# Optimization experiments

Hardware: AMD Instinct MI355X
Metric: run time of the kernel (lower is better)

The kernel has to match this reference:

```python
import jax, jax.numpy as jnp
import numpy as np

TEMPERATURE = 0.05
SINKHORN_ITERS = 10


def setup_inputs() -> dict:
    key = jax.random.key(0)
    ks = jax.random.split(key, 6)
    N, D, E = 4096, 300, 32768
    x = jax.random.normal(ks[0], (N, D), dtype=jnp.float32)
    W1 = jax.random.normal(ks[1], (D, D), dtype=jnp.float32) * 0.05
    b1 = jax.random.normal(ks[2], (D,), dtype=jnp.float32) * 0.01
    W2 = jax.random.normal(ks[3], (D, D), dtype=jnp.float32) * 0.05
    b2 = jax.random.normal(ks[4], (D,), dtype=jnp.float32) * 0.01
    edge_index = jax.random.randint(ks[5], (2, E), 0, N, dtype=jnp.int64)
    return {"x": x, "W1": W1, "b1": b1, "W2": W2, "b2": b2,
            "edge_index": edge_index}


def _sinkhorn(dot):
    # dot: [N, N]; batch dim of 1 in the original collapses away.
    in_size = dot.shape[0]
    out_size = dot.shape[1]
    K = jnp.exp(dot)
    v = jnp.ones((out_size,), dtype=K.dtype)
    a = jnp.asarray(out_size / in_size, dtype=K.dtype)
    u = jnp.ones((in_size,), dtype=K.dtype)
    for _ in range(SINKHORN_ITERS):
        u = a / (K @ v)            # [N]
        v = 1.0 / (u @ K)          # [N]
    return u[:, None] * (K * v[None, :])  # [N, N] coupling


def reference(x, W1, b1, W2, b2, edge_index):
    N = x.shape[0]
    # projector: Linear -> ReLU -> Linear
    out = jax.nn.relu(x @ W1 + b1) @ W2 + b2
    # L2 normalize rows (torch F.normalize with eps=1e-12)
    norm = jnp.maximum(jnp.linalg.norm(out, axis=1, keepdims=True), 1e-12)
    node_features = out / norm
    logits = (node_features @ node_features.T) / TEMPERATURE  # [N, N]
    log_probs = jax.nn.log_softmax(logits, axis=1)
    # Sinkhorn coupling computed under no_grad in the original
    coupling = jax.lax.stop_gradient(_sinkhorn(logits))
    loss = -jnp.mean(jnp.sum(coupling * log_probs, axis=1))
    # dense 2-hop adjacency target
    src, dst = edge_index[0], edge_index[1]
    adj = jnp.zeros((N, N), dtype=jnp.float32).at[src, dst].set(1.0)
    adj = adj + jnp.eye(N, dtype=jnp.float32)
    adj2 = ((adj @ adj) > 0).astype(jnp.float32)
    targets = adj2 / jnp.sum(adj2, axis=0, keepdims=True)
    loss = loss + (-jnp.mean(jnp.sum(targets * log_probs, axis=1)))
    return loss
```

## Files before the change

### kernel.cpp

```cpp
#include <hip/hip_runtime.h>
#include <cstdint>
#include <cstddef>

#define N 4096
#define D 300
#define KP 320
#define INV_T 20.0f
#define SK_ITERS 10
#define NTILE 528

typedef __attribute__((ext_vector_type(8))) short bf16x8;
typedef __attribute__((ext_vector_type(4))) float f32x4;
typedef __attribute__((ext_vector_type(8))) unsigned short ushort8;

__device__ inline void tile_decode(int blk, int& bi, int& bj) {
  int lin = (blk & 7) * 66 + (blk >> 3);
  int a = 0;
  while (lin >= 32 - a) { lin -= 32 - a; ++a; }
  bi = a; bj = a + lin;
}

__global__ void zero_u32(unsigned int* __restrict__ p, int n) {
  int i = blockIdx.x * 256 + threadIdx.x;
  int stride = gridDim.x * 256;
  for (; i < n; i += stride) p[i] = 0u;
}

__global__ __launch_bounds__(320) void mlp_gemm(const float* __restrict__ A,
                                                const float* __restrict__ B,
                                                const float* __restrict__ bias,
                                                float* __restrict__ C, int relu) {
  __shared__ __align__(16) float As[4][304];
  int r0 = blockIdx.x * 4;
  for (int idx = threadIdx.x; idx < 4 * 300; idx += 320) {
    int r = idx / 300, k = idx - r * 300;
    As[r][k] = A[(size_t)(r0 + r) * D + k];
  }
  __syncthreads();
  int c = threadIdx.x;
  if (c < D) {
    float acc[4] = {0, 0, 0, 0};
    for (int k = 0; k < D; k += 4) {
      float b0 = B[(size_t)(k + 0) * D + c];
      float b1 = B[(size_t)(k + 1) * D + c];
      float b2 = B[(size_t)(k + 2) * D + c];
      float b3 = B[(size_t)(k + 3) * D + c];
#pragma unroll
      for (int r = 0; r < 4; ++r) {
        const float4 a4 = *reinterpret_cast<const float4*>(&As[r][k]);
        acc[r] += a4.x * b0 + a4.y * b1 + a4.z * b2 + a4.w * b3;
      }
    }
#pragma unroll
    for (int r = 0; r < 4; ++r) {
      float o = acc[r] + bias[c];
      if (relu) o = fmaxf(o, 0.0f);
      C[(size_t)(r0 + r) * D + c] = o;
    }
  }
}

__device__ inline unsigned short bf16_rne(float v) {
  unsigned int u = __float_as_uint(v);
  unsigned int r = u + 0x7fffu + ((u >> 16) & 1u);
  return (unsigned short)(r >> 16);
}

__global__ __launch_bounds__(64) void normalize_split(const float* __restrict__ in,
                                                      unsigned short* __restrict__ fhi,
                                                      unsigned short* __restrict__ flo) {
  int row = blockIdx.x;
  const float* r = in + (size_t)row * D;
  float ss = 0.0f;
  for (int c = threadIdx.x; c < D; c += 64) {
    float v = r[c];
    ss += v * v;
  }
  for (int o = 32; o > 0; o >>= 1) ss += __shfl_down(ss, o);
  ss = __shfl(ss, 0);
  float inv = 1.0f / fmaxf(sqrtf(ss), 1e-12f);
  for (int c = threadIdx.x; c < KP; c += 64) {
    float v = (c < D) ? r[c] * inv : 0.0f;
    unsigned short h = bf16_rne(v);
    float hf = __uint_as_float((unsigned int)h << 16);
    unsigned short lo = bf16_rne(v - hf);
    fhi[(size_t)row * KP + c] = h;
    flo[(size_t)row * KP + c] = lo;
  }
}

__global__ __launch_bounds__(256) void logits_mfma(const unsigned short* __restrict__ fhi,
                                                   const unsigned short* __restrict__ flo,
                                                   float* __restrict__ logits) {
  __shared__ unsigned short smem[4 * 128 * 32];
  int bi, bj;
  tile_decode(blockIdx.x, bi, bj);
  int row0 = bi * 128, col0 = bj * 128;
  int tid = threadIdx.x;
  int w = tid >> 6, l = tid & 63;
  int wr = w >> 1, wc = w & 1;
  f32x4 acc[4][4] = {};

  for (int k0 = 0; k0 < KP; k0 += 32) {
    ushort8 stg[8];
#pragma unroll
    for (int t = 0; t < 8; ++t) {
      int c = t * 256 + tid;
      int b = c >> 9, i = c & 511, row = i >> 2, k16 = i & 3;
      const unsigned short* base = (b & 1) ? flo : fhi;
      int blk = (b < 2) ? row0 : col0;
      stg[t] = *reinterpret_cast<const ushort8*>(
          &base[(size_t)(blk + row) * KP + k0 + k16 * 8]);
    }
    __syncthreads();
#pragma unroll
    for (int t = 0; t < 8; ++t) {
      int c = t * 256 + tid;
      *reinterpret_cast<ushort8*>(&smem[c * 8]) = stg[t];
    }
    __syncthreads();

    bf16x8 ah[4], al[4], bh[4], bl[4];
#pragma unroll
    for (int m = 0; m < 4; ++m) {
      int off = (wr * 64 + m * 16 + (l & 15)) * 32 + (l >> 4) * 8;
      ah[m] = *reinterpret_cast<const bf16x8*>(&smem[0 * 4096 + off]);
      al[m] = *reinterpret_cast<const bf16x8*>(&smem[1 * 4096 + off]);
    }
#pragma unroll
    for (int n = 0; n < 4; ++n) {
      int off = (wc * 64 + n * 16 + (l & 15)) * 32 + (l >> 4) * 8;
      bh[n] = *reinterpret_cast<const bf16x8*>(&smem[2 * 4096 + off]);
      bl[n] = *reinterpret_cast<const bf16x8*>(&smem[3 * 4096 + off]);
    }
#pragma unroll
    for (int m = 0; m < 4; ++m)
#pragma unroll
      for (int n = 0; n < 4; ++n) {
        acc[m][n] = __builtin_amdgcn_mfma_f32_16x16x32_bf16(ah[m], bh[n], acc[m][n], 0, 0, 0);
        acc[m][n] = __builtin_amdgcn_mfma_f32_16x16x32_bf16(ah[m], bl[n], acc[m][n], 0, 0, 0);
        acc[m][n] = __builtin_amdgcn_mfma_f32_16x16x32_bf16(al[m], bh[n], acc[m][n], 0, 0, 0);
      }
  }

  int rb = row0 + wr * 64, cb = col0 + wc * 64;
  int rsub = (l >> 4) * 4, csub = l & 15;
#pragma unroll
  for (int m = 0; m < 4; ++m) {
#pragma unroll
    for (int n = 0; n < 4; ++n) {
      int col = cb + n * 16 + csub;
#pragma unroll
      for (int j = 0; j < 4; ++j) {
        logits[(size_t)(rb + m * 16 + rsub + j) * N + col] = acc[m][n][j] * INV_T;
      }
    }
  }
}

__global__ __launch_bounds__(256) void sk_tile(const float* __restrict__ logits,
                                               const float* __restrict__ vin,
                                               float* __restrict__ pr) {
  __shared__ float red[16][8][17];
  int bi, bj;
  tile_decode(blockIdx.x, bi, bj);
  int row0 = bi * 128, col0 = bj * 128;
  int t = threadIdx.x, ty = t >> 4, tx = t & 15;
  int r0 = ty * 8, c0 = tx * 8;
  float vc[8];
  *reinterpret_cast<float4*>(&vc[0]) = *reinterpret_cast<const float4*>(&vin[col0 + c0]);
  *reinterpret_cast<float4*>(&vc[4]) = *reinterpret_cast<const float4*>(&vin[col0 + c0 + 4]);
  float cs[8] = {};
#pragma unroll
  for (int i = 0; i < 8; ++i) {
    const float* lp = logits + (size_t)(row0 + r0 + i) * N + col0 + c0;
    float4 q0 = *reinterpret_cast<const float4*>(lp);
    float4 q1 = *reinterpret_cast<const float4*>(lp + 4);
    float vri = vin[row0 + r0 + i];
    float e[8] = {__expf(q0.x), __expf(q0.y), __expf(q0.z), __expf(q0.w),
                  __expf(q1.x), __expf(q1.y), __expf(q1.z), __expf(q1.w)};
    float rs = 0.f;
#pragma unroll
    for (int j = 0; j < 8; ++j) { rs += e[j] * vc[j]; cs[j] += e[j] * vri; }
    red[ty][i][tx] = rs;
  }
  __syncthreads();
  if (t < 128) {
    float s = 0.f;
#pragma unroll
    for (int x = 0; x < 16; ++x) s += red[t >> 3][t & 7][x];
    pr[((size_t)bi * 32 + bj) * 128 + t] = s;
  }
  if (bi != bj) {
    __syncthreads();
#pragma unroll
    for (int j = 0; j < 8; ++j) red[tx][j][ty] = cs[j];
    __syncthreads();
    if (t < 128) {
      float s = 0.f;
#pragma unroll
      for (int y = 0; y < 16; ++y) s += red[t >> 3][t & 7][y];
      pr[((size_t)bj * 32 + bi) * 128 + t] = s;
    }
  }
}

__global__ __launch_bounds__(256) void sk_reduce(const float* __restrict__ pr,
                                                 float* __restrict__ vout,
                                                 float* __restrict__ lse, int store_lse) {
  int i = blockIdx.x * 256 + threadIdx.x;
  int a = i >> 7, ri = i & 127;
  float tot = 0.f;
#pragma unroll
  for (int s = 0; s < 32; ++s) tot += pr[((size_t)a * 32 + s) * 128 + ri];
  vout[i] = 1.0f / tot;
  if (store_lse) lse[i] = logf(tot);
}

__global__ __launch_bounds__(256) void loss1_tile(const float* __restrict__ logits,
                                                  const float* __restrict__ v,
                                                  float* __restrict__ pr0,
                                                  float* __restrict__ pr1) {
  __shared__ float red[16][8][17];
  int bi, bj;
  tile_decode(blockIdx.x, bi, bj);
  int row0 = bi * 128, col0 = bj * 128;
  int t = threadIdx.x, ty = t >> 4, tx = t & 15;
  int r0 = ty * 8, c0 = tx * 8;
  float vc[8];
  *reinterpret_cast<float4*>(&vc[0]) = *reinterpret_cast<const float4*>(&v[col0 + c0]);
  *reinterpret_cast<float4*>(&vc[4]) = *reinterpret_cast<const float4*>(&v[col0 + c0 + 4]);
  float cs0[8] = {}, cs1[8] = {};
  float rs0a[8], rs1a[8];
#pragma unroll
  for (int i = 0; i < 8; ++i) {
    const float* lp = logits + (size_t)(row0 + r0 + i) * N + col0 + c0;
    float4 q0 = *reinterpret_cast<const float4*>(lp);
    float4 q1 = *reinterpret_cast<const float4*>(lp + 4);
    float ql[8] = {q0.x, q0.y, q0.z, q0.w, q1.x, q1.y, q1.z, q1.w};
    float vri = v[row0 + r0 + i];
    float rs0 = 0.f, rs1 = 0.f;
#pragma unroll
    for (int j = 0; j < 8; ++j) {
      float l = ql[j];
      float e = __expf(l);
      float wv = e * vc[j];
      rs0 += wv; rs1 += wv * l;
      cs0[j] += e * vri; cs1[j] += e * vri * l;
    }
    rs0a[i] = rs0; rs1a[i] = rs1;
  }
  size_t up = ((size_t)bi * 32 + bj) * 128;
  size_t dn = ((size_t)bj * 32 + bi) * 128;
#pragma unroll
  for (int i = 0; i < 8; ++i) red[ty][i][tx] = rs0a[i];
  __syncthreads();
  if (t < 128) {
    float s = 0.f;
#pragma unroll
    for (int x = 0; x < 16; ++x) s += red[t >> 3][t & 7][x];
    pr0[up + t] = s;
  }
  __syncthreads();
#pragma unroll
  for (int i = 0; i < 8; ++i) red[ty][i][tx] = rs1a[i];
  __syncthreads();
  if (t < 128) {
    float s = 0.f;
#pragma unroll
    for (int x = 0; x < 16; ++x) s += red[t >> 3][t & 7][x];
    pr1[up + t] = s;
  }
  if (bi != bj) {
    __syncthreads();
#pragma unroll
    for (int j = 0; j < 8; ++j) red[tx][j][ty] = cs0[j];
    __syncthreads();
    if (t < 128) {
      float s = 0.f;
#pragma unroll
      for (int y = 0; y < 16; ++y) s += red[t >> 3][t & 7][y];
      pr0[dn + t] = s;
    }
    __syncthreads();
#pragma unroll
    for (int j = 0; j < 8; ++j) red[tx][j][ty] = cs1[j];
    __syncthreads();
    if (t < 128) {
      float s = 0.f;
#pragma unroll
      for (int y = 0; y < 16; ++y) s += red[t >> 3][t & 7][y];
      pr1[dn + t] = s;
    }
  }
}

__global__ __launch_bounds__(256) void loss1_reduce(const float* __restrict__ pr0,
                                                    const float* __restrict__ pr1,
                                                    const float* __restrict__ u,
                                                    const float* __restrict__ lse,
                                                    double* __restrict__ term1) {
  int i = blockIdx.x * 256 + threadIdx.x;
  int a = i >> 7, ri = i & 127;
  double s0 = 0.0, s1 = 0.0;
#pragma unroll
  for (int s = 0; s < 32; ++s) {
    s0 += (double)pr0[((size_t)a * 32 + s) * 128 + ri];
    s1 += (double)pr1[((size_t)a * 32 + s) * 128 + ri];
  }
  term1[i] = (double)u[i] * (s1 - (double)lse[i] * s0);
}

__global__ void init_ones(float* v) {
  int i = blockIdx.x * 256 + threadIdx.x;
  if (i < N) v[i] = 1.0f;
}

__global__ void build_adj(const int* __restrict__ ei, int E,
                          unsigned int* __restrict__ adjmask, int* __restrict__ deg) {
  int t = blockIdx.x * 256 + threadIdx.x;
  if (t < E) {
    int s = ei[t] & (N - 1), d = ei[E + t] & (N - 1);
    atomicOr(&adjmask[(size_t)s * 128 + (d >> 5)], 1u << (d & 31));
    atomicAdd(&deg[s], 1);
  }
  if (t < N) atomicOr(&adjmask[(size_t)t * 128 + (t >> 5)], 1u << (t & 31));
}

__global__ __launch_bounds__(1024) void scan_deg(const int* __restrict__ deg,
                                                 int* __restrict__ offs,
                                                 int* __restrict__ cursor) {
  __shared__ int part[1024];
  int tid = threadIdx.x;
  int base = tid * 4;
  int l0 = deg[base + 0], l1 = deg[base + 1], l2 = deg[base + 2], l3 = deg[base + 3];
  part[tid] = l0 + l1 + l2 + l3;
  __syncthreads();
  for (int d = 1; d < 1024; d <<= 1) {
    int v = (tid >= d) ? part[tid - d] : 0;
    __syncthreads();
    part[tid] += v;
    __syncthreads();
  }
  int run = (tid > 0) ? part[tid - 1] : 0;
  offs[base + 0] = run; cursor[base + 0] = run; run += l0;
  offs[base + 1] = run; cursor[base + 1] = run; run += l1;
  offs[base + 2] = run; cursor[base + 2] = run; run += l2;
  offs[base + 3] = run; cursor[base + 3] = run;
}

__global__ void scatter_edges(const int* __restrict__ ei, int E,
                              int* __restrict__ cursor, int* __restrict__ neigh) {
  int t = blockIdx.x * 256 + threadIdx.x;
  if (t < E) {
    int s = ei[t] & (N - 1), d = ei[E + t] & (N - 1);
    int slot = atomicAdd(&cursor[s], 1);
    neigh[slot] = d;
  }
}

__global__ __launch_bounds__(128) void adj2_kernel(const unsigned int* __restrict__ adjmask,
                                                   const int* __restrict__ offs,
                                                   const int* __restrict__ deg,
                                                   const int* __restrict__ neigh,
                                                   unsigned int* __restrict__ adj2,
                                                   int* __restrict__ colcount) {
  int i = blockIdx.x, w = threadIdx.x;
  unsigned int acc = adjmask[(size_t)i * 128 + w];
  int o = offs[i], dg = deg[i];
  for (int n = 0; n < dg; ++n) {
    int k = neigh[o + n];
    acc |= adjmask[(size_t)k * 128 + w];
  }
  adj2[(size_t)i * 128 + w] = acc;
  unsigned int m = acc;
  while (m) {
    int b = __ffs(m) - 1;
    m &= m - 1;
    atomicAdd(&colcount[w * 32 + b], 1);
  }
}

__global__ __launch_bounds__(128) void loss2_kernel(const unsigned int* __restrict__ adj2,
                                                    const int* __restrict__ colcount,
                                                    const float* __restrict__ logits,
                                                    const float* __restrict__ lse,
                                                    double* __restrict__ term2) {
  __shared__ float sb[2], sb2[2];
  int i = blockIdx.x, w = threadIdx.x;
  unsigned int m = adj2[(size_t)i * 128 + w];
  float s = 0.0f, sc = 0.0f;
  while (m) {
    int b = __ffs(m) - 1;
    m &= m - 1;
    int j = w * 32 + b;
    float lij = (j < i) ? logits[(size_t)j * N + i] : logits[(size_t)i * N + j];
    float ic = 1.0f / (float)colcount[j];
    s += ic * lij;
    sc += ic;
  }
  for (int o = 32; o > 0; o >>= 1) {
    s += __shfl_down(s, o);
    sc += __shfl_down(sc, o);
  }
  int lane = w & 63, wid = w >> 6;
  if (lane == 0) { sb[wid] = s; sb2[wid] = sc; }
  __syncthreads();
  if (w == 0)
    term2[i] = (double)(sb[0] + sb[1]) - (double)lse[i] * (double)(sb2[0] + sb2[1]);
}

__global__ __launch_bounds__(256) void final_reduce(const double* __restrict__ term1,
                                                    const double* __restrict__ term2,
                                                    float* __restrict__ out) {
  __shared__ double sb[4];
  double s = 0.0;
  for (int i = threadIdx.x; i < N; i += 256) s += term1[i] + term2[i];
  for (int o = 32; o > 0; o >>= 1) s += __shfl_down(s, o);
  int lane = threadIdx.x & 63, wid = threadIdx.x >> 6;
  if (lane == 0) sb[wid] = s;
  __syncthreads();
  if (threadIdx.x == 0) out[0] = (float)(-(sb[0] + sb[1] + sb[2] + sb[3]) / (double)N);
}

extern "C" void kernel_launch(void* const* d_in, const int* in_sizes, int n_in,
                              void* d_out, int out_size, void* d_ws, size_t ws_size,
                              hipStream_t stream) {
  const float* x  = (const float*)d_in[0];
  const float* W1 = (const float*)d_in[1];
  const float* b1 = (const float*)d_in[2];
  const float* W2 = (const float*)d_in[3];
  const float* b2 = (const float*)d_in[4];
  const int* ei = (const int*)d_in[5];
  int E = in_sizes[5] / 2;
  float* outp = (float*)d_out;

  char* w = (char*)d_ws;
  float* logits = (float*)w;  w += (size_t)N * N * 4;
  float* h      = (float*)w;  w += (size_t)N * D * 4;
  float* o2     = (float*)w;  w += (size_t)N * D * 4;
  unsigned short* fhi = (unsigned short*)w; w += (size_t)N * KP * 2;
  unsigned short* flo = (unsigned short*)w; w += (size_t)N * KP * 2;
  float* vecA   = (float*)w;  w += 16384;
  float* vecB   = (float*)w;  w += 16384;
  float* lse    = (float*)w;  w += 16384;
  double* term1 = (double*)w; w += 32768;
  double* term2 = (double*)w; w += 32768;
  float* pr0    = (float*)w;  w += 32 * 32 * 128 * 4;
  float* pr1    = (float*)w;  w += 32 * 32 * 128 * 4;
  unsigned int* adjmask = (unsigned int*)w; w += (size_t)N * 128 * 4;
  int* colcount = (int*)w;    w += 16384;
  int* deg      = (int*)w;    w += 16384;
  int zcount = N * 128 + 4096 + 4096;
  unsigned int* adj2 = (unsigned int*)w; w += (size_t)N * 128 * 4;
  int* offs   = (int*)w;      w += 16384;
  int* cursor = (int*)w;      w += 16384;
  int* neigh  = (int*)w;      w += (size_t)E * 4;

  zero_u32<<<512, 256, 0, stream>>>(adjmask, zcount);

  mlp_gemm<<<N / 4, 320, 0, stream>>>(x, W1, b1, h, 1);
  mlp_gemm<<<N / 4, 320, 0, stream>>>(h, W2, b2, o2, 0);
  normalize_split<<<N, 64, 0, stream>>>(o2, fhi, flo);
  logits_mfma<<<NTILE, 256, 0, stream>>>(fhi, flo, logits);
  init_ones<<<(N + 255) / 256, 256, 0, stream>>>(vecA);

  int gmax = (E > N ? E : N);
  build_adj<<<(gmax + 255) / 256, 256, 0, stream>>>(ei, E, adjmask, deg);
  scan_deg<<<1, 1024, 0, stream>>>(deg, offs, cursor);
  scatter_edges<<<(E + 255) / 256, 256, 0, stream>>>(ei, E, cursor, neigh);

  for (int it = 0; it < SK_ITERS; ++it) {
    sk_tile<<<NTILE, 256, 0, stream>>>(logits, vecA, pr0);
    sk_reduce<<<N / 256, 256, 0, stream>>>(pr0, vecB, lse, it == 0 ? 1 : 0);
    sk_tile<<<NTILE, 256, 0, stream>>>(logits, vecB, pr0);
    sk_reduce<<<N / 256, 256, 0, stream>>>(pr0, vecA, lse, 0);
  }
  loss1_tile<<<NTILE, 256, 0, stream>>>(logits, vecA, pr0, pr1);
  loss1_reduce<<<N / 256, 256, 0, stream>>>(pr0, pr1, vecB, lse, term1);

  adj2_kernel<<<N, 128, 0, stream>>>(adjmask, offs, deg, neigh, adj2, colcount);
  loss2_kernel<<<N, 128, 0, stream>>>(adj2, colcount, logits, lse, term2);

  final_reduce<<<1, 256, 0, stream>>>(term1, term2, outp);
}
```

Baseline: 385.8 us.

## Precompute bf16 exp(K) in logits kernel and fuse Sinkhorn tile/reduce via atomics

The logits GEMM epilogue now also writes exp(logits) as a bf16 matrix. Each Sinkhorn half-step becomes one fused kernel: it reads the half-size bf16 K instead of fp32 logits with repeated exp, inverts the previous totals in-kernel, and accumulates row and column sums with atomicAdd into rotating buffers. This drops the separate reduce launches and cuts memory traffic per pass. The trade-offs are bf16 precision loss in the Sinkhorn scaling, float atomics that make the sums nondeterministic, and an extra N*N*2-byte write in the GEMM.

```diff
diff --git a/kernel.cpp b/kernel.cpp
--- a/kernel.cpp
+++ b/kernel.cpp
@@ -91,7 +91,8 @@
 
 __global__ __launch_bounds__(256) void logits_mfma(const unsigned short* __restrict__ fhi,
                                                    const unsigned short* __restrict__ flo,
-                                                   float* __restrict__ logits) {
+                                                   float* __restrict__ logits,
+                                                   unsigned short* __restrict__ kexp) {
   __shared__ unsigned short smem[4 * 128 * 32];
   int bi, bj;
   tile_decode(blockIdx.x, bi, bj);
@@ -152,44 +153,73 @@
       int col = cb + n * 16 + csub;
 #pragma unroll
       for (int j = 0; j < 4; ++j) {
-        logits[(size_t)(rb + m * 16 + rsub + j) * N + col] = acc[m][n][j] * INV_T;
+        size_t idx = (size_t)(rb + m * 16 + rsub + j) * N + col;
+        float lv = acc[m][n][j] * INV_T;
+        logits[idx] = lv;
+        kexp[idx] = bf16_rne(__expf(lv));
       }
     }
   }
 }
 
-__global__ __launch_bounds__(256) void sk_tile(const float* __restrict__ logits,
-                                               const float* __restrict__ vin,
-                                               float* __restrict__ pr) {
+__global__ __launch_bounds__(256) void sk_fused(const unsigned short* __restrict__ kexp,
+                                                const float* __restrict__ totprev,
+                                                float* __restrict__ totcur,
+                                                float* __restrict__ totnext,
+                                                float* __restrict__ lse,
+                                                int first, int write_lse) {
   __shared__ float red[16][8][17];
+  __shared__ float vrow[128], vcol[128];
   int bi, bj;
   tile_decode(blockIdx.x, bi, bj);
   int row0 = bi * 128, col0 = bj * 128;
-  int t = threadIdx.x, ty = t >> 4, tx = t & 15;
+  int t = threadIdx.x;
+  if (t < 8) {
+    int zb = blockIdx.x * 8 + t;
+    if (zb < N) totnext[zb] = 0.f;
+  }
+  if (first) {
+    if (t < 128) vrow[t] = 1.f;
+    else vcol[t - 128] = 1.f;
+  } else {
+    if (t < 128) {
+      float tt = totprev[row0 + t];
+      vrow[t] = 1.f / tt;
+      if (write_lse && bi == bj) lse[row0 + t] = logf(tt);
+    } else {
+      vcol[t - 128] = 1.f / totprev[col0 + (t - 128)];
+    }
+  }
+  __syncthreads();
+  int ty = t >> 4, tx = t & 15;
   int r0 = ty * 8, c0 = tx * 8;
   float vc[8];
-  *reinterpret_cast<float4*>(&vc[0]) = *reinterpret_cast<const float4*>(&vin[col0 + c0]);
-  *reinterpret_cast<float4*>(&vc[4]) = *reinterpret_cast<const float4*>(&vin[col0 + c0 + 4]);
+#pragma unroll
+  for (int j = 0; j < 8; ++j) vc[j] = vcol[c0 + j];
   float cs[8] = {};
+  float rsa[8];
 #pragma unroll
   for (int i = 0; i < 8; ++i) {
-    const float* lp = logits + (size_t)(row0 + r0 + i) * N + col0 + c0;
-    float4 q0 = *reinterpret_cast<const float4*>(lp);
-    float4 q1 = *reinterpret_cast<const float4*>(lp + 4);
-    float vri = vin[row0 + r0 + i];
-    float e[8] = {__expf(q0.x), __expf(q0.y), __expf(q0.z), __expf(q0.w),
-                  __expf(q1.x), __expf(q1.y), __expf(q1.z), __expf(q1.w)};
+    const ushort8 kv = *reinterpret_cast<const ushort8*>(
+        &kexp[(size_t)(row0 + r0 + i) * N + col0 + c0]);
+    float vri = vrow[r0 + i];
     float rs = 0.f;
 #pragma unroll
-    for (int j = 0; j < 8; ++j) { rs += e[j] * vc[j]; cs[j] += e[j] * vri; }
-    red[ty][i][tx] = rs;
-  }
+    for (int j = 0; j < 8; ++j) {
+      float e = __uint_as_float((unsigned int)(unsigned short)kv[j] << 16);
+      rs += e * vc[j];
+      cs[j] += e * vri;
+    }
+    rsa[i] = rs;
+  }
+#pragma unroll
+  for (int i = 0; i < 8; ++i) red[ty][i][tx] = rsa[i];
   __syncthreads();
   if (t < 128) {
     float s = 0.f;
 #pragma unroll
     for (int x = 0; x < 16; ++x) s += red[t >> 3][t & 7][x];
-    pr[((size_t)bi * 32 + bj) * 128 + t] = s;
+    atomicAdd(&totcur[row0 + t], s);
   }
   if (bi != bj) {
     __syncthreads();
@@ -200,21 +230,16 @@
       float s = 0.f;
 #pragma unroll
       for (int y = 0; y < 16; ++y) s += red[t >> 3][t & 7][y];
-      pr[((size_t)bj * 32 + bi) * 128 + t] = s;
-    }
-  }
-}
-
-__global__ __launch_bounds__(256) void sk_reduce(const float* __restrict__ pr,
-                                                 float* __restrict__ vout,
-                                                 float* __restrict__ lse, int store_lse) {
+      atomicAdd(&totcur[col0 + t], s);
+    }
+  }
+}
+
+__global__ void invert2(const float* __restrict__ a, const float* __restrict__ b,
+                        float* __restrict__ ua, float* __restrict__ vb) {
   int i = blockIdx.x * 256 + threadIdx.x;
-  int a = i >> 7, ri = i & 127;
-  float tot = 0.f;
-#pragma unroll
-  for (int s = 0; s < 32; ++s) tot += pr[((size_t)a * 32 + s) * 128 + ri];
-  vout[i] = 1.0f / tot;
-  if (store_lse) lse[i] = logf(tot);
+  ua[i] = 1.f / a[i];
+  vb[i] = 1.f / b[i];
 }
 
 __global__ __launch_bounds__(256) void loss1_tile(const float* __restrict__ logits,
@@ -309,11 +334,6 @@
     s1 += (double)pr1[((size_t)a * 32 + s) * 128 + ri];
   }
   term1[i] = (double)u[i] * (s1 - (double)lse[i] * s0);
-}
-
-__global__ void init_ones(float* v) {
-  int i = blockIdx.x * 256 + threadIdx.x;
-  if (i < N) v[i] = 1.0f;
 }
 
 __global__ void build_adj(const int* __restrict__ ei, int E,
@@ -437,6 +457,7 @@
 
   char* w = (char*)d_ws;
   float* logits = (float*)w;  w += (size_t)N * N * 4;
+  unsigned short* kexp = (unsigned short*)w; w += (size_t)N * N * 2;
   float* h      = (float*)w;  w += (size_t)N * D * 4;
   float* o2     = (float*)w;  w += (size_t)N * D * 4;
   unsigned short* fhi = (unsigned short*)w; w += (size_t)N * KP * 2;
@@ -448,34 +469,39 @@
   double* term2 = (double*)w; w += 32768;
   float* pr0    = (float*)w;  w += 32 * 32 * 128 * 4;
   float* pr1    = (float*)w;  w += 32 * 32 * 128 * 4;
+  float* sb0 = (float*)w;     w += 16384;
+  float* sb1 = (float*)w;     w += 16384;
+  float* sb2 = (float*)w;     w += 16384;
   unsigned int* adjmask = (unsigned int*)w; w += (size_t)N * 128 * 4;
   int* colcount = (int*)w;    w += 16384;
   int* deg      = (int*)w;    w += 16384;
-  int zcount = N * 128 + 4096 + 4096;
+  int zcount = 3 * N + N * 128 + 4096 + 4096;
   unsigned int* adj2 = (unsigned int*)w; w += (size_t)N * 128 * 4;
   int* offs   = (int*)w;      w += 16384;
   int* cursor = (int*)w;      w += 16384;
   int* neigh  = (int*)w;      w += (size_t)E * 4;
 
-  zero_u32<<<512, 256, 0, stream>>>(adjmask, zcount);
+  zero_u32<<<512, 256, 0, stream>>>((unsigned int*)sb0, zcount);
 
   mlp_gemm<<<N / 4, 320, 0, stream>>>(x, W1, b1, h, 1);
   mlp_gemm<<<N / 4, 320, 0, stream>>>(h, W2, b2, o2, 0);
   normalize_split<<<N, 64, 0, stream>>>(o2, fhi, flo);
-  logits_mfma<<<NTILE, 256, 0, stream>>>(fhi, flo, logits);
-  init_ones<<<(N + 255) / 256, 256, 0, stream>>>(vecA);
+  logits_mfma<<<NTILE, 256, 0, stream>>>(fhi, flo, logits, kexp);
 
   int gmax = (E > N ? E : N);
   build_adj<<<(gmax + 255) / 256, 256, 0, stream>>>(ei, E, adjmask, deg);
   scan_deg<<<1, 1024, 0, stream>>>(deg, offs, cursor);
   scatter_edges<<<(E + 255) / 256, 256, 0, stream>>>(ei, E, cursor, neigh);
 
-  for (int it = 0; it < SK_ITERS; ++it) {
-    sk_tile<<<NTILE, 256, 0, stream>>>(logits, vecA, pr0);
-    sk_reduce<<<N / 256, 256, 0, stream>>>(pr0, vecB, lse, it == 0 ? 1 : 0);
-    sk_tile<<<NTILE, 256, 0, stream>>>(logits, vecB, pr0);
-    sk_reduce<<<N / 256, 256, 0, stream>>>(pr0, vecA, lse, 0);
-  }
+  float* bufs[3] = {sb0, sb1, sb2};
+  for (int p = 0; p < 2 * SK_ITERS; ++p) {
+    sk_fused<<<NTILE, 256, 0, stream>>>(kexp,
+        p == 0 ? sb0 : bufs[(p - 1) % 3],
+        bufs[p % 3], bufs[(p + 1) % 3], lse,
+        p == 0 ? 1 : 0, p == 1 ? 1 : 0);
+  }
+  invert2<<<N / 256, 256, 0, stream>>>(bufs[0], bufs[1], vecA, vecB);
+
   loss1_tile<<<NTILE, 256, 0, stream>>>(logits, vecA, pr0, pr1);
   loss1_reduce<<<N / 256, 256, 0, stream>>>(pr0, pr1, vecB, lse, term1);
 
```

Result: faster. 320.6 us (-16.9%).
